# Optimization experiments

Measured on AMD Instinct MI355X. Metric: run time of the kernel, lower is better.

## Reference

```python
import jax, jax.numpy as jnp
import numpy as np

B, S, D, H, E, K, F = 1, 1024, 1024, 16, 8, 2, 4096


def setup_inputs() -> dict:
    key = jax.random.key(0)
    ks = jax.random.split(key, 8)
    n = lambda k, shape, sc: (jax.random.normal(k, shape, dtype=jnp.float32) * sc)
    return {
        "x": n(ks[0], (B, S, D), 1.0),
        "w_qkv": n(ks[1], (D, 3 * D), D ** -0.5),
        "w_o": n(ks[2], (D, D), D ** -0.5),
        "g1": jnp.ones((D,), jnp.float32),
        "b1": jnp.zeros((D,), jnp.float32),
        "wg": n(ks[3], (D, E), D ** -0.5),
        "w1": n(ks[4], (E, D, F), D ** -0.5),
        "bb1": jnp.zeros((E, F), jnp.float32),
        "w2": n(ks[5], (E, F, D), F ** -0.5),
        "bb2": jnp.zeros((E, D), jnp.float32),
        "g2": jnp.ones((D,), jnp.float32),
        "b2": jnp.zeros((D,), jnp.float32),
    }


def layernorm(x, g, b, eps=1e-5):
    m = x.mean(-1, keepdims=True)
    v = ((x - m) ** 2).mean(-1, keepdims=True)
    return (x - m) * jax.lax.rsqrt(v + eps) * g + b


def reference(x, w_qkv, w_o, g1, b1, wg, w1, bb1, w2, bb2, g2, b2):
    b, s, d = x.shape
    hd = d // H
    # --- multi-head causal self-attention ---
    qkv = x @ w_qkv  # [b,s,3d]
    q, k, v = jnp.split(qkv, 3, axis=-1)
    to_heads = lambda t: t.reshape(b, s, H, hd).transpose(0, 2, 1, 3)  # [b,h,s,hd]
    q, k, v = to_heads(q), to_heads(k), to_heads(v)
    scores = jnp.einsum("bhqd,bhkd->bhqk", q, k) / jnp.sqrt(jnp.float32(hd))
    causal = jnp.tril(jnp.ones((s, s), bool))
    scores = jnp.where(causal, scores, jnp.finfo(scores.dtype).min)
    attn = jax.nn.softmax(scores, axis=-1)
    o = jnp.einsum("bhqk,bhkd->bhqd", attn, v)
    o = o.transpose(0, 2, 1, 3).reshape(b, s, d) @ w_o
    # --- add & norm ---
    h = layernorm(x + o, g1, b1)
    # --- MoE FFN: softmax router, top-k, renormalized combine ---
    probs = jax.nn.softmax(h @ wg, axis=-1)  # [b,s,E]
    topv, topi = jax.lax.top_k(probs, K)
    topv = topv / topv.sum(-1, keepdims=True)
    w = (topv[..., None] * jax.nn.one_hot(topi, E, dtype=h.dtype)).sum(-2)  # [b,s,E]
    h1 = jax.nn.gelu(jnp.einsum("bsd,edf->ebsf", h, w1) + bb1[:, None, None, :])
    y = jnp.einsum("ebsf,efd->ebsd", h1, w2) + bb2[:, None, None, :]
    moe = jnp.einsum("ebsd,bse->bsd", y, w)
    # --- residual + norm of MoE block ---
    return layernorm(h + moe, g2, b2)
```

## Files before the change

kernel.cpp:

```cpp
#include <hip/hip_runtime.h>
#include <hip/hip_bf16.h>
#include <math.h>

#define SEQ 1024
#define DIM 1024
#define NH  16
#define NE  8
#define FF  4096

typedef float f32x4 __attribute__((ext_vector_type(4)));
typedef float f32x2 __attribute__((ext_vector_type(2)));
typedef short short8 __attribute__((ext_vector_type(8)));
typedef short s16x4 __attribute__((ext_vector_type(4)));

#define WAIT_VM(N) asm volatile("s_waitcnt vmcnt(" #N ")" ::: "memory")

__device__ __forceinline__ ushort f2bf(float f) {
  union { float f; unsigned u; } v; v.f = f;
  unsigned r = v.u + 0x7FFF + ((v.u >> 16) & 1);
  return (ushort)(r >> 16);
}
__device__ __forceinline__ float bf2f(ushort h) {
  union { unsigned u; float f; } v; v.u = ((unsigned)h) << 16;
  return v.f;
}

__device__ __forceinline__ float gelu_tanh(float x) {
  return 0.5f * x * (1.f + tanhf(0.7978845608028654f * (x + 0.044715f * x * x * x)));
}
__device__ __forceinline__ float gelu_fast(float x) {
  float u = 1.5957691216057308f * (x + 0.044715f * x * x * x);
  return x / (1.f + __expf(-u));
}

__device__ __forceinline__ void gl2lds16(const void* g, void* l) {
  __builtin_amdgcn_global_load_lds(
      (const __attribute__((address_space(1))) unsigned int*)g,
      (__attribute__((address_space(3))) unsigned int*)l, 16, 0, 0);
}

__global__ __launch_bounds__(256) void wconv_kernel(
    const float* __restrict__ wq, const float* __restrict__ wo,
    ushort* __restrict__ wqT, ushort* __restrict__ wqTl,
    ushort* __restrict__ woT, ushort* __restrict__ woTl) {
  __shared__ __align__(16) ushort th[64 * 64];
  __shared__ __align__(16) ushort tl[64 * 64];
  int z = blockIdx.z, t = threadIdx.x;
  const float* src; ushort* dh; ushort* dl; int R, C, r0, c0;
  if (z == 0) {
    src = wq; dh = wqT; dl = wqTl;
    R = DIM; C = 3 * DIM; r0 = blockIdx.y * 64; c0 = blockIdx.x * 64;
  } else {
    if (blockIdx.x >= 16) return;
    src = wo; dh = woT; dl = woTl;
    R = DIM; C = DIM; r0 = blockIdx.y * 64; c0 = blockIdx.x * 64;
  }
  int ry = (t >> 4) * 4;
  int cx = (t & 15) * 4;
  f32x4 v[4];
#pragma unroll
  for (int j = 0; j < 4; j++)
    v[j] = *(const f32x4*)&src[(size_t)(r0 + ry + j) * C + c0 + cx];
#pragma unroll
  for (int i = 0; i < 4; i++) {
    int trow = cx + i;
    int o = trow * 64 + (((ry >> 3) ^ (trow & 7)) << 3) + (ry & 7);
    ushort uh[4], ul[4];
#pragma unroll
    for (int j = 0; j < 4; j++) {
      float f = v[j][i];
      ushort hh = f2bf(f);
      uh[j] = hh;
      ul[j] = f2bf(f - bf2f(hh));
    }
    *(s16x4*)&th[o] = *(const s16x4*)uh;
    *(s16x4*)&tl[o] = *(const s16x4*)ul;
  }
  __syncthreads();
  int tr = t >> 2, tc = (t & 3) * 16;
  int b0 = (tc >> 3) ^ (tr & 7);
  int b1 = ((tc >> 3) + 1) ^ (tr & 7);
  size_t dbase = (size_t)(c0 + tr) * R + r0 + tc;
  short8 u0 = *(const short8*)&th[tr * 64 + b0 * 8];
  short8 u1 = *(const short8*)&th[tr * 64 + b1 * 8];
  *(short8*)&dh[dbase] = u0;
  *(short8*)&dh[dbase + 8] = u1;
  short8 l0 = *(const short8*)&tl[tr * 64 + b0 * 8];
  short8 l1 = *(const short8*)&tl[tr * 64 + b1 * 8];
  *(short8*)&dl[dbase] = l0;
  *(short8*)&dl[dbase + 8] = l1;
}

__global__ __launch_bounds__(256) void bfsplit_kernel(const float* __restrict__ in,
                                                      ushort* __restrict__ oh,
                                                      ushort* __restrict__ ol) {
  int i = (blockIdx.x * 256 + threadIdx.x) * 4;
  f32x4 v = *(const f32x4*)&in[i];
  ushort h[4], l[4];
#pragma unroll
  for (int j = 0; j < 4; j++) { h[j] = f2bf(v[j]); l[j] = f2bf(v[j] - bf2f(h[j])); }
  *(s16x4*)&oh[i] = *(const s16x4*)h;
  *(s16x4*)&ol[i] = *(const s16x4*)l;
}

#define MM_FEXP_LOAD(ra0v, ra1v, rb0v, rb1v, rb2v, rb3v, T)            \
  { int _ko = (T) * 32;                                                \
    ra0v = *(const short8*)(aG[0] + _ko);                              \
    ra1v = *(const short8*)(aG[1] + _ko);                              \
    rb0v = *(const f32x4*)(bG + (size_t)(_ko + 0) * N);                \
    rb1v = *(const f32x4*)(bG + (size_t)(_ko + 1) * N);                \
    rb2v = *(const f32x4*)(bG + (size_t)(_ko + 2) * N);                \
    rb3v = *(const f32x4*)(bG + (size_t)(_ko + 3) * N); }

#define MM_FEXP_STAGE(buf, ra0v, ra1v, rb0v, rb1v, rb2v, rb3v)         \
  { *(short8*)&As[buf][aw[0]] = ra0v;                                  \
    *(short8*)&As[buf][aw[1]] = ra1v;                                  \
    _Pragma("unroll")                                                  \
    for (int i = 0; i < 4; i++) {                                      \
      ushort u[4];                                                     \
      u[0] = f2bf(rb0v[i]); u[1] = f2bf(rb1v[i]);                      \
      u[2] = f2bf(rb2v[i]); u[3] = f2bf(rb3v[i]);                      \
      *(s16x4*)&Bs[buf][(nb * 4 + i) * 40 + bslot * 4] = *(const s16x4*)u; } }

#define MM_FEXP_MFMA(buf)                                              \
  { short8 af[4], bf[4];                                               \
    _Pragma("unroll")                                                  \
    for (int mi = 0; mi < 4; mi++) af[mi] = *(const short8*)&As[buf][aro[mi]]; \
    _Pragma("unroll")                                                  \
    for (int ni = 0; ni < 4; ni++) bf[ni] = *(const short8*)&Bs[buf][bro[ni]]; \
    _Pragma("unroll")                                                  \
    for (int mi = 0; mi < 4; mi++)                                     \
      _Pragma("unroll")                                                \
      for (int ni = 0; ni < 4; ni++)                                   \
        acc[mi][ni] = __builtin_amdgcn_mfma_f32_16x16x32_bf16(af[mi], bf[ni], acc[mi][ni], 0, 0, 0); }

template <int EPI, int KSPLIT>
__global__ __launch_bounds__(256) void mm_fexp(
    const ushort* __restrict__ A, const float* __restrict__ Bf,
    const float* __restrict__ bias, void* __restrict__ Cout,
    const int* __restrict__ tok, const int* __restrict__ offcnt,
    int N, int K)
{
  int zz = blockIdx.z;
  int e  = (KSPLIT > 1) ? (zz & (NE - 1)) : zz;
  int ks = (KSPLIT > 1) ? (zz >> 3) : 0;
  int off = offcnt[e], cnt = offcnt[NE + e];
  int m0 = blockIdx.y * 128;
  if (m0 >= cnt) return;
  int n0 = blockIdx.x * 128;
  const float* Bp = Bf + (size_t)e * K * N;
  const int Kc = K / KSPLIT, kbase = ks * Kc;

  __shared__ __align__(16) ushort As[2][128 * 32];
  __shared__ __align__(16) ushort Bs[2][128 * 40];

  int t = threadIdx.x, lane = t & 63, w = t >> 6, wr = w >> 1, wc = w & 1;

  const ushort* aG[2]; int aw[2];
#pragma unroll
  for (int c = 0; c < 2; c++) {
    int gid = w * 128 + c * 64 + lane;
    int m = gid >> 2, p = gid & 3;
    int kg = p ^ ((m >> 1) & 3);
    int mc = m0 + m; if (mc > cnt - 1) mc = cnt - 1;
    int arow = tok ? tok[off + mc] : (off + mc);
    aG[c] = A + (size_t)arow * K + kbase + kg * 8;
    aw[c] = gid * 8;
  }

  int kb = t >> 5, nb = t & 31;
  const float* bG = Bp + (size_t)(kbase + kb * 4) * N + n0 + nb * 4;
  int bslot = kb ^ ((nb & 3) << 1);

  int aro[4], bro[4];
#pragma unroll
  for (int mi = 0; mi < 4; mi++) {
    int m = wr * 64 + mi * 16 + (lane & 15);
    aro[mi] = (m * 4 + ((lane >> 4) ^ ((m >> 1) & 3))) * 8;
  }
#pragma unroll
  for (int ni = 0; ni < 4; ni++) {
    int n = wc * 64 + ni * 16 + (lane & 15);
    bro[ni] = n * 40 + ((((lane >> 4) * 2) ^ (((n >> 2) & 3) << 1))) * 4;
  }

  f32x4 acc[4][4] = {};
  const int nt = Kc / 32;

  short8 raA0, raA1, raB0, raB1;
  f32x4 rbA0, rbA1, rbA2, rbA3, rbB0, rbB1, rbB2, rbB3;
  MM_FEXP_LOAD(raA0, raA1, rbA0, rbA1, rbA2, rbA3, 0);
  MM_FEXP_LOAD(raB0, raB1, rbB0, rbB1, rbB2, rbB3, 1);

  for (int tt = 0; tt < nt; tt += 2) {
    MM_FEXP_STAGE(0, raA0, raA1, rbA0, rbA1, rbA2, rbA3);
    if (tt + 2 < nt) MM_FEXP_LOAD(raA0, raA1, rbA0, rbA1, rbA2, rbA3, tt + 2);
    asm volatile("s_waitcnt lgkmcnt(0)" ::: "memory");
    __builtin_amdgcn_sched_barrier(0);
    __builtin_amdgcn_s_barrier();
    MM_FEXP_MFMA(0);
    MM_FEXP_STAGE(1, raB0, raB1, rbB0, rbB1, rbB2, rbB3);
    if (tt + 3 < nt) MM_FEXP_LOAD(raB0, raB1, rbB0, rbB1, rbB2, rbB3, tt + 3);
    asm volatile("s_waitcnt lgkmcnt(0)" ::: "memory");
    __builtin_amdgcn_sched_barrier(0);
    __builtin_amdgcn_s_barrier();
    MM_FEXP_MFMA(1);
  }

  const float* biasp = (EPI == 3) ? nullptr : bias + (size_t)e * N;
  float* Cp = (float*)Cout + (size_t)ks * 2048 * N;
#pragma unroll
  for (int mi = 0; mi < 4; mi++) {
#pragma unroll
    for (int j = 0; j < 4; j++) {
      int grow = m0 + wr * 64 + mi * 16 + (lane >> 4) * 4 + j;
      if (grow >= cnt) continue;
      size_t rbase = (size_t)(off + grow) * N;
#pragma unroll
      for (int ni = 0; ni < 4; ni++) {
        int gcol = n0 + wc * 64 + ni * 16 + (lane & 15);
        float v = acc[mi][ni][j];
        if (EPI == 1) ((ushort*)Cout)[rbase + gcol] = f2bf(gelu_fast(v + biasp[gcol]));
        else          Cp[rbase + gcol] = v;
      }
    }
  }
}

#undef MM_FEXP_LOAD
#undef MM_FEXP_STAGE
#undef MM_FEXP_MFMA

__global__ __launch_bounds__(256) void mm_split(
    const ushort* __restrict__ Ah, const ushort* __restrict__ Al,
    const ushort* __restrict__ Bh, const ushort* __restrict__ Bl,
    float* __restrict__ C, int N, int K)
{
  int m0 = blockIdx.y * 128;
  int n0 = blockIdx.x * 128;

  __shared__ __align__(16) ushort Ahs[2][4096], Als[2][4096];
  __shared__ __align__(16) ushort Bhs[2][4096], Bls[2][4096];

  int t = threadIdx.x, lane = t & 63, w = t >> 6, wr = w >> 1, wc = w & 1;

  const ushort *aGh[2], *aGl[2], *bGh[2], *bGl[2];
  int lofs[2];
#pragma unroll
  for (int c = 0; c < 2; c++) {
    int gid = w * 128 + c * 64 + lane;
    int m = gid >> 2, p = gid & 3;
    int kg = p ^ ((m >> 1) & 3);
    aGh[c] = Ah + (size_t)(m0 + m) * K + kg * 8;
    aGl[c] = Al + (size_t)(m0 + m) * K + kg * 8;
    bGh[c] = Bh + (size_t)(n0 + m) * K + kg * 8;
    bGl[c] = Bl + (size_t)(n0 + m) * K + kg * 8;
    lofs[c] = (w * 128 + c * 64) * 8;
  }

  int aro[4], bro[4];
#pragma unroll
  for (int mi = 0; mi < 4; mi++) {
    int m = wr * 64 + mi * 16 + (lane & 15);
    aro[mi] = (m * 4 + ((lane >> 4) ^ ((m >> 1) & 3))) * 8;
  }
#pragma unroll
  for (int ni = 0; ni < 4; ni++) {
    int n = wc * 64 + ni * 16 + (lane & 15);
    bro[ni] = (n * 4 + ((lane >> 4) ^ ((n >> 1) & 3))) * 8;
  }

  f32x4 acc[4][4] = {};
  const int nt = K / 32;

#pragma unroll
  for (int c = 0; c < 2; c++) {
    gl2lds16(aGh[c], &Ahs[0][lofs[c]]); gl2lds16(aGl[c], &Als[0][lofs[c]]);
    gl2lds16(bGh[c], &Bhs[0][lofs[c]]); gl2lds16(bGl[c], &Bls[0][lofs[c]]);
  }
  if (nt > 1) {
#pragma unroll
    for (int c = 0; c < 2; c++) {
      gl2lds16(aGh[c] + 32, &Ahs[1][lofs[c]]); gl2lds16(aGl[c] + 32, &Als[1][lofs[c]]);
      gl2lds16(bGh[c] + 32, &Bhs[1][lofs[c]]); gl2lds16(bGl[c] + 32, &Bls[1][lofs[c]]);
    }
  }

  for (int tt = 0; tt < nt; tt++) {
    if (tt + 1 < nt) WAIT_VM(8); else WAIT_VM(0);
    __builtin_amdgcn_s_barrier();
    int b = tt & 1;
    short8 ah[4], al_[4], bh[4], bl_[4];
#pragma unroll
    for (int mi = 0; mi < 4; mi++) {
      ah[mi] = *(const short8*)&Ahs[b][aro[mi]];
      al_[mi] = *(const short8*)&Als[b][aro[mi]];
    }
#pragma unroll
    for (int ni = 0; ni < 4; ni++) {
      bh[ni] = *(const short8*)&Bhs[b][bro[ni]];
      bl_[ni] = *(const short8*)&Bls[b][bro[ni]];
    }
#pragma unroll
    for (int mi = 0; mi < 4; mi++)
#pragma unroll
      for (int ni = 0; ni < 4; ni++) {
        acc[mi][ni] = __builtin_amdgcn_mfma_f32_16x16x32_bf16(al_[mi], bh[ni], acc[mi][ni], 0, 0, 0);
        acc[mi][ni] = __builtin_amdgcn_mfma_f32_16x16x32_bf16(ah[mi], bl_[ni], acc[mi][ni], 0, 0, 0);
        acc[mi][ni] = __builtin_amdgcn_mfma_f32_16x16x32_bf16(ah[mi], bh[ni], acc[mi][ni], 0, 0, 0);
      }
    asm volatile("s_waitcnt lgkmcnt(0)" ::: "memory");
    __builtin_amdgcn_sched_barrier(0);
    __builtin_amdgcn_s_barrier();
    if (tt + 2 < nt) {
      int ko = (tt + 2) * 32;
#pragma unroll
      for (int c = 0; c < 2; c++) {
        gl2lds16(aGh[c] + ko, &Ahs[b][lofs[c]]); gl2lds16(aGl[c] + ko, &Als[b][lofs[c]]);
        gl2lds16(bGh[c] + ko, &Bhs[b][lofs[c]]); gl2lds16(bGl[c] + ko, &Bls[b][lofs[c]]);
      }
    }
  }

#pragma unroll
  for (int mi = 0; mi < 4; mi++)
#pragma unroll
    for (int j = 0; j < 4; j++) {
      int grow = m0 + wr * 64 + mi * 16 + (lane >> 4) * 4 + j;
      size_t rbase = (size_t)grow * N;
#pragma unroll
      for (int ni = 0; ni < 4; ni++) {
        int gcol = n0 + wc * 64 + ni * 16 + (lane & 15);
        C[rbase + gcol] = acc[mi][ni][j];
      }
    }
}

template <int EPI, int SPLIT>
__global__ __launch_bounds__(256) void mm_bf16(
    const float* __restrict__ A, const float* __restrict__ B,
    const float* __restrict__ bias, float* __restrict__ C,
    const int* __restrict__ tok, const int* __restrict__ offcnt,
    int M, int N, int K)
{
  int e = blockIdx.z;
  int off = 0, cnt = M;
  if (offcnt) { off = offcnt[e]; cnt = offcnt[NE + e]; }
  int m0 = blockIdx.y * 128;
  if (m0 >= cnt) return;
  const float* Bp = B + (size_t)e * K * N;
  const float* biasp = (EPI == 0) ? nullptr : bias + (size_t)e * N;
  int n0 = blockIdx.x * 128;

  __shared__ __align__(16) ushort As[(SPLIT + 1) * 128 * 32];
  __shared__ __align__(16) ushort Bs[(SPLIT + 1) * 128 * 32];

  int t = threadIdx.x;
  int lane = t & 63;
  int w = t >> 6, wr = w >> 1, wc = w & 1;

  const float* aptr[2];
  int aws[2];
  for (int i = 0; i < 2; i++) {
    int mr = i * 64 + (t >> 2);
    int mc = m0 + mr; if (mc > cnt - 1) mc = cnt - 1;
    int arow = tok ? tok[off + mc] : (off + mc);
    aptr[i] = A + (size_t)arow * K + (t & 3) * 8;
    aws[i] = mr * 32 + (t & 3) * 8;
  }

  int bn = t >> 1, bkh = (t & 1) * 16;
  const float* bptr = Bp + (size_t)bkh * N + n0 + bn;
  int bws0 = bn * 32 + 8 * (((bkh >> 3) + 0) ^ (bn & 3));
  int bws1 = bn * 32 + 8 * (((bkh >> 3) + 1) ^ (bn & 3));

  int aro[4], bro[4];
#pragma unroll
  for (int mi = 0; mi < 4; mi++)
    aro[mi] = (wr * 64 + mi * 16 + (lane & 15)) * 32 + (lane >> 4) * 8;
#pragma unroll
  for (int ni = 0; ni < 4; ni++) {
    int n = wc * 64 + ni * 16 + (lane & 15);
    bro[ni] = n * 32 + 8 * ((lane >> 4) ^ (n & 3));
  }

  f32x4 acc[4][4] = {};

  for (int k0 = 0; k0 < K; k0 += 32) {
#pragma unroll
    for (int i = 0; i < 2; i++) {
      f32x4 v0 = *(const f32x4*)(aptr[i] + k0);
      f32x4 v1 = *(const f32x4*)(aptr[i] + k0 + 4);
      ushort uh[8], ul[8];
#pragma unroll
      for (int j = 0; j < 4; j++) {
        float f0 = v0[j], f1 = v1[j];
        ushort h0 = f2bf(f0), h1 = f2bf(f1);
        uh[j] = h0; uh[4 + j] = h1;
        if (SPLIT) { ul[j] = f2bf(f0 - bf2f(h0)); ul[4 + j] = f2bf(f1 - bf2f(h1)); }
      }
      *(short8*)&As[aws[i]] = *(const short8*)uh;
      if (SPLIT) *(short8*)&As[4096 + aws[i]] = *(const short8*)ul;
    }
    {
      const float* bp = bptr + (size_t)k0 * N;
      ushort uh[16], ul[16];
#pragma unroll
      for (int i = 0; i < 16; i++) {
        float f = bp[(size_t)i * N];
        ushort h = f2bf(f);
        uh[i] = h;
        if (SPLIT) ul[i] = f2bf(f - bf2f(h));
      }
      *(short8*)&Bs[bws0] = *(const short8*)&uh[0];
      *(short8*)&Bs[bws1] = *(const short8*)&uh[8];
      if (SPLIT) {
        *(short8*)&Bs[4096 + bws0] = *(const short8*)&ul[0];
        *(short8*)&Bs[4096 + bws1] = *(const short8*)&ul[8];
      }
    }
    __syncthreads();
    short8 afh[4], bfh[4], afl[4], bfl[4];
#pragma unroll
    for (int mi = 0; mi < 4; mi++) {
      afh[mi] = *(const short8*)&As[aro[mi]];
      if (SPLIT) afl[mi] = *(const short8*)&As[4096 + aro[mi]];
    }
#pragma unroll
    for (int ni = 0; ni < 4; ni++) {
      bfh[ni] = *(const short8*)&Bs[bro[ni]];
      if (SPLIT) bfl[ni] = *(const short8*)&Bs[4096 + bro[ni]];
    }
#pragma unroll
    for (int mi = 0; mi < 4; mi++)
#pragma unroll
      for (int ni = 0; ni < 4; ni++) {
        if (SPLIT) {
          acc[mi][ni] = __builtin_amdgcn_mfma_f32_16x16x32_bf16(afl[mi], bfh[ni], acc[mi][ni], 0, 0, 0);
          acc[mi][ni] = __builtin_amdgcn_mfma_f32_16x16x32_bf16(afh[mi], bfl[ni], acc[mi][ni], 0, 0, 0);
        }
        acc[mi][ni] = __builtin_amdgcn_mfma_f32_16x16x32_bf16(afh[mi], bfh[ni], acc[mi][ni], 0, 0, 0);
      }
    __syncthreads();
  }

#pragma unroll
  for (int mi = 0; mi < 4; mi++) {
#pragma unroll
    for (int j = 0; j < 4; j++) {
      int grow = m0 + wr * 64 + mi * 16 + (lane >> 4) * 4 + j;
      if (grow >= cnt) continue;
      size_t rbase = (size_t)(off + grow) * N;
#pragma unroll
      for (int ni = 0; ni < 4; ni++) {
        int gcol = n0 + wc * 64 + ni * 16 + (lane & 15);
        float v = acc[mi][ni][j];
        if (EPI >= 1) v += biasp[gcol];
        if (EPI == 1) v = gelu_tanh(v);
        C[rbase + gcol] = v;
      }
    }
  }
}

__device__ __forceinline__ int vidx(int d, int key) {
  return d * 64 + ((((key >> 3) ^ (d & 7)) << 3) | (key & 7));
}

__global__ __launch_bounds__(256, 1) void attn_mfma(const float* __restrict__ qkv,
                                                    float* __restrict__ opart,
                                                    float* __restrict__ ml) {
  const int qb = blockIdx.x;
  const int ch = blockIdx.y;
  const int head = blockIdx.z;
  const int q0 = qb * 128;
  const int t = threadIdx.x;
  const int lane = t & 63, w = t >> 6;
  const int g = lane >> 4, l4 = lane & 15;

  __shared__ __align__(16) ushort Kh[64 * 64], Kl[64 * 64];
  __shared__ __align__(16) ushort Vh[64 * 64], Vl[64 * 64];
  __shared__ __align__(16) ushort Ph[4][32 * 72], Pl[4][32 * 72];

  short8 qh[2][2], ql[2][2];
#pragma unroll
  for (int mi = 0; mi < 2; mi++)
#pragma unroll
    for (int ks = 0; ks < 2; ks++) {
      int row = q0 + w * 32 + mi * 16 + l4;
      const float* qp = qkv + (size_t)row * 3072 + head * 64 + ks * 32 + g * 8;
      f32x4 a = *(const f32x4*)qp;
      f32x4 b4 = *(const f32x4*)(qp + 4);
      ushort uh[8], ul_[8];
#pragma unroll
      for (int j = 0; j < 4; j++) {
        ushort h0 = f2bf(a[j]), h1 = f2bf(b4[j]);
        uh[j] = h0; uh[4 + j] = h1;
        ul_[j] = f2bf(a[j] - bf2f(h0)); ul_[4 + j] = f2bf(b4[j] - bf2f(h1));
      }
      qh[mi][ks] = *(const short8*)uh;
      ql[mi][ks] = *(const short8*)ul_;
    }

  float m_s[2][4], l_s[2][4];
  f32x4 O[2][4] = {};
#pragma unroll
  for (int mi = 0; mi < 2; mi++)
#pragma unroll
    for (int j = 0; j < 4; j++) { m_s[mi][j] = -1e30f; l_s[mi][j] = 0.f; }

  const int kt_beg = ch ? (qb + 1) : 0;
  const int kt_end = ch ? 2 * (qb + 1) : (qb + 1);
  for (int kt = kt_beg; kt < kt_end; kt++) {
    const int kv0 = kt * 64;
    __syncthreads();
    {
      int key = t >> 2;
      int dblk = (t & 3) * 16;
      const float* kp = qkv + (size_t)(kv0 + key) * 3072 + 1024 + head * 64 + dblk;
      const float* vp = kp + 1024;
      f32x4 k0 = *(const f32x4*)kp, k1 = *(const f32x4*)(kp + 4),
            k2 = *(const f32x4*)(kp + 8), k3 = *(const f32x4*)(kp + 12);
      f32x4 v0 = *(const f32x4*)vp, v1 = *(const f32x4*)(vp + 4),
            v2 = *(const f32x4*)(vp + 8), v3 = *(const f32x4*)(vp + 12);
      float kf[16] = {k0[0],k0[1],k0[2],k0[3], k1[0],k1[1],k1[2],k1[3],
                      k2[0],k2[1],k2[2],k2[3], k3[0],k3[1],k3[2],k3[3]};
      float vf[16] = {v0[0],v0[1],v0[2],v0[3], v1[0],v1[1],v1[2],v1[3],
                      v2[0],v2[1],v2[2],v2[3], v3[0],v3[1],v3[2],v3[3]};
#pragma unroll
      for (int half = 0; half < 2; half++) {
        int d8 = (dblk >> 3) + half;
        int idx = key * 64 + ((d8 ^ (key & 7)) << 3);
        ushort uh[8], ul_[8];
#pragma unroll
        for (int j = 0; j < 8; j++) {
          float f = kf[half * 8 + j];
          ushort h = f2bf(f);
          uh[j] = h; ul_[j] = f2bf(f - bf2f(h));
        }
        *(short8*)&Kh[idx] = *(const short8*)uh;
        *(short8*)&Kl[idx] = *(const short8*)ul_;
      }
#pragma unroll
      for (int i = 0; i < 16; i++) {
        int d = dblk + i;
        int idx = vidx(d, key);
        float f = vf[i];
        ushort h = f2bf(f);
        Vh[idx] = h; Vl[idx] = f2bf(f - bf2f(h));
      }
    }
    __syncthreads();

    if (kv0 <= q0 + w * 32 + 31) {
      f32x4 S[2][4] = {};
#pragma unroll
      for (int ks = 0; ks < 2; ks++) {
        short8 kbh[4], kbl[4];
#pragma unroll
        for (int ni = 0; ni < 4; ni++) {
          int key = ni * 16 + l4;
          int d8 = ks * 4 + g;
          int idx = key * 64 + ((d8 ^ (key & 7)) << 3);
          kbh[ni] = *(const short8*)&Kh[idx];
          kbl[ni] = *(const short8*)&Kl[idx];
        }
#pragma unroll
        for (int mi = 0; mi < 2; mi++)
#pragma unroll
          for (int ni = 0; ni < 4; ni++) {
            S[mi][ni] = __builtin_amdgcn_mfma_f32_16x16x32_bf16(ql[mi][ks], kbh[ni], S[mi][ni], 0, 0, 0);
            S[mi][ni] = __builtin_amdgcn_mfma_f32_16x16x32_bf16(qh[mi][ks], kbl[ni], S[mi][ni], 0, 0, 0);
            S[mi][ni] = __builtin_amdgcn_mfma_f32_16x16x32_bf16(qh[mi][ks], kbh[ni], S[mi][ni], 0, 0, 0);
          }
      }
#pragma unroll
      for (int mi = 0; mi < 2; mi++) {
        int rowb = q0 + w * 32 + mi * 16 + g * 4;
        float mx[4] = {-1e30f, -1e30f, -1e30f, -1e30f};
#pragma unroll
        for (int ni = 0; ni < 4; ni++) {
          int col = kv0 + ni * 16 + l4;
#pragma unroll
          for (int j = 0; j < 4; j++) {
            float s = S[mi][ni][j] * 0.125f;
            if (col > rowb + j) s = -1e30f;
            S[mi][ni][j] = s;
            mx[j] = fmaxf(mx[j], s);
          }
        }
#pragma unroll
        for (int j = 0; j < 4; j++) {
#pragma unroll
          for (int msk = 8; msk; msk >>= 1) mx[j] = fmaxf(mx[j], __shfl_xor(mx[j], msk));
          float mn = fmaxf(m_s[mi][j], mx[j]);
          float sc = __expf(m_s[mi][j] - mn);
          m_s[mi][j] = mn;
          l_s[mi][j] *= sc;
#pragma unroll
          for (int df = 0; df < 4; df++) O[mi][df][j] *= sc;
        }
        float ps[4] = {0.f, 0.f, 0.f, 0.f};
#pragma unroll
        for (int ni = 0; ni < 4; ni++)
#pragma unroll
          for (int j = 0; j < 4; j++) {
            float p = __expf(S[mi][ni][j] - m_s[mi][j]);
            ps[j] += p;
            int rl = mi * 16 + g * 4 + j, cl = ni * 16 + l4;
            ushort h = f2bf(p);
            Ph[w][rl * 72 + cl] = h;
            Pl[w][rl * 72 + cl] = f2bf(p - bf2f(h));
          }
#pragma unroll
        for (int j = 0; j < 4; j++) {
#pragma unroll
          for (int msk = 8; msk; msk >>= 1) ps[j] += __shfl_xor(ps[j], msk);
          l_s[mi][j] += ps[j];
        }
      }
      asm volatile("s_waitcnt lgkmcnt(0)" ::: "memory");
      __builtin_amdgcn_sched_barrier(0);
#pragma unroll
      for (int ks = 0; ks < 2; ks++) {
        short8 pah[2], pal[2], vbh[4], vbl[4];
#pragma unroll
        for (int mi = 0; mi < 2; mi++) {
          int idx = (mi * 16 + l4) * 72 + ks * 32 + g * 8;
          pah[mi] = *(const short8*)&Ph[w][idx];
          pal[mi] = *(const short8*)&Pl[w][idx];
        }
#pragma unroll
        for (int df = 0; df < 4; df++) {
          int d = df * 16 + l4;
          int k8 = ks * 4 + g;
          int idx = d * 64 + ((k8 ^ (d & 7)) << 3);
          vbh[df] = *(const short8*)&Vh[idx];
          vbl[df] = *(const short8*)&Vl[idx];
        }
#pragma unroll
        for (int mi = 0; mi < 2; mi++)
#pragma unroll
          for (int df = 0; df < 4; df++) {
            O[mi][df] = __builtin_amdgcn_mfma_f32_16x16x32_bf16(pal[mi], vbh[df], O[mi][df], 0, 0, 0);
            O[mi][df] = __builtin_amdgcn_mfma_f32_16x16x32_bf16(pah[mi], vbl[df], O[mi][df], 0, 0, 0);
            O[mi][df] = __builtin_amdgcn_mfma_f32_16x16x32_bf16(pah[mi], vbh[df], O[mi][df], 0, 0, 0);
          }
      }
    }
  }

#pragma unroll
  for (int mi = 0; mi < 2; mi++)
#pragma unroll
    for (int j = 0; j < 4; j++) {
      int row = q0 + w * 32 + mi * 16 + g * 4 + j;
      if (l4 == 0) {
        float* mlp = ml + (((size_t)ch * NH + head) * SEQ + row) * 2;
        mlp[0] = m_s[mi][j];
        mlp[1] = l_s[mi][j];
      }
#pragma unroll
      for (int df = 0; df < 4; df++)
        opart[(size_t)ch * (SEQ * DIM) + (size_t)row * DIM + head * 64 + df * 16 + l4] =
            O[mi][df][j];
    }
}

__global__ __launch_bounds__(256) void attn_combine(const float* __restrict__ opart,
                                                    const float* __restrict__ ml,
                                                    float* __restrict__ o) {
  int row = blockIdx.x, t = threadIdx.x;
  int d0 = t * 4;
  int head = d0 >> 6;
  const float* p0 = ml + (((size_t)0 * NH + head) * SEQ + row) * 2;
  const float* p1 = ml + (((size_t)1 * NH + head) * SEQ + row) * 2;
  float m0 = p0[0], l0 = p0[1], m1 = p1[0], l1 = p1[1];
  float M = fmaxf(m0, m1);
  float w0 = __expf(m0 - M), w1 = __expf(m1 - M);
  float inv = 1.f / (l0 * w0 + l1 * w1);
  f32x4 O0 = *(const f32x4*)&opart[(size_t)row * DIM + d0];
  f32x4 O1 = *(const f32x4*)&opart[(size_t)(SEQ * DIM) + (size_t)row * DIM + d0];
  f32x4 r;
#pragma unroll
  for (int j = 0; j < 4; j++) r[j] = (O0[j] * w0 + O1[j] * w1) * inv;
  *(f32x4*)&o[(size_t)row * DIM + d0] = r;
}

__device__ float block_reduce_256(float v, float* red, int t) {
  red[t] = v; __syncthreads();
  for (int st = 128; st > 0; st >>= 1) {
    if (t < st) red[t] += red[t + st];
    __syncthreads();
  }
  float r = red[0];
  __syncthreads();
  return r;
}

__global__ __launch_bounds__(256) void addln_kernel(const float* __restrict__ x,
                                                    const float* __restrict__ r,
                                                    const float* __restrict__ g,
                                                    const float* __restrict__ b,
                                                    float* __restrict__ out,
                                                    ushort* __restrict__ outb) {
  __shared__ float red[256];
  int row = blockIdx.x, t = threadIdx.x;
  float vals[4];
  float s = 0.f;
  for (int i = 0; i < 4; i++) {
    int d = t + i * 256;
    vals[i] = x[(size_t)row * DIM + d] + r[(size_t)row * DIM + d];
    s += vals[i];
  }
  float mean = block_reduce_256(s, red, t) * (1.f / DIM);
  float vs = 0.f;
  for (int i = 0; i < 4; i++) { float d = vals[i] - mean; vs += d * d; }
  float var = block_reduce_256(vs, red, t) * (1.f / DIM);
  float inv = rsqrtf(var + 1e-5f);
  for (int i = 0; i < 4; i++) {
    int d = t + i * 256;
    float v = (vals[i] - mean) * inv * g[d] + b[d];
    out[(size_t)row * DIM + d] = v;
    if (outb) outb[(size_t)row * DIM + d] = f2bf(v);
  }
}

__global__ __launch_bounds__(256) void router_kernel(const float* __restrict__ h,
                                                     const float* __restrict__ wg,
                                                     int* __restrict__ topi,
                                                     float* __restrict__ topw) {
  __shared__ float red[NE][256];
  int tkn = blockIdx.x, t = threadIdx.x;
  float acc[NE] = {};
  for (int i = 0; i < 4; i++) {
    int d = t + i * 256;
    float hv = h[(size_t)tkn * DIM + d];
    const float* wr = wg + (size_t)d * NE;
    for (int e = 0; e < NE; e++) acc[e] += hv * wr[e];
  }
  for (int e = 0; e < NE; e++) red[e][t] = acc[e];
  __syncthreads();
  for (int st = 128; st > 0; st >>= 1) {
    if (t < st)
      for (int e = 0; e < NE; e++) red[e][t] += red[e][t + st];
    __syncthreads();
  }
  if (t == 0) {
    float l[NE];
    for (int e = 0; e < NE; e++) l[e] = red[e][0];
    int i0 = 0;
    for (int e = 1; e < NE; e++) if (l[e] > l[i0]) i0 = e;
    int i1 = -1;
    for (int e = 0; e < NE; e++) {
      if (e == i0) continue;
      if (i1 < 0 || l[e] > l[i1]) i1 = e;
    }
    float p1 = __expf(l[i1] - l[i0]);
    float inv = 1.f / (1.f + p1);
    topi[tkn * 2] = i0; topi[tkn * 2 + 1] = i1;
    topw[tkn * 2] = inv; topw[tkn * 2 + 1] = p1 * inv;
  }
}

__global__ __launch_bounds__(1024) void compact_kernel(const int* __restrict__ topi,
                                                       int* __restrict__ tok,
                                                       int* __restrict__ assign_row,
                                                       int* __restrict__ offcnt) {
  __shared__ int scan[1024];
  __shared__ int sbase;
  int t = threadIdx.x;
  if (t == 0) sbase = 0;
  __syncthreads();
  for (int e = 0; e < NE; e++) {
    int which = -1;
    if (topi[t * 2] == e) which = 0;
    else if (topi[t * 2 + 1] == e) which = 1;
    scan[t] = (which >= 0) ? 1 : 0;
    __syncthreads();
    for (int s2 = 1; s2 < 1024; s2 <<= 1) {
      int add = (t >= s2) ? scan[t - s2] : 0;
      __syncthreads();
      scan[t] += add;
      __syncthreads();
    }
    int incl = scan[t];
    int total = scan[1023];
    int base = sbase;
    if (which >= 0) {
      int pos = base + incl - 1;
      tok[pos] = t;
      assign_row[t * 2 + which] = pos;
    }
    if (t == 0) { offcnt[e] = base; offcnt[NE + e] = total; }
    __syncthreads();
    if (t == 0) sbase = base + total;
    __syncthreads();
  }
}

template <int KS>
__global__ __launch_bounds__(256) void final_ln_kernel(const float* __restrict__ h,
                                                       const float* __restrict__ y,
                                                       const int* __restrict__ assign_row,
                                                       const float* __restrict__ topw,
                                                       const int* __restrict__ topi,
                                                       const float* __restrict__ bb2,
                                                       const float* __restrict__ g,
                                                       const float* __restrict__ b,
                                                       float* __restrict__ out) {
  __shared__ float red[256];
  int row = blockIdx.x, t = threadIdx.x;
  int r0 = assign_row[row * 2], r1 = assign_row[row * 2 + 1];
  float w0 = topw[row * 2], w1 = topw[row * 2 + 1];
  float vals[4];
  float s = 0.f;
  for (int i = 0; i < 4; i++) {
    int d = t + i * 256;
    float acc0 = 0.f, acc1 = 0.f;
#pragma unroll
    for (int p = 0; p < KS; p++) {
      acc0 += y[(size_t)p * 2048 * DIM + (size_t)r0 * DIM + d];
      acc1 += y[(size_t)p * 2048 * DIM + (size_t)r1 * DIM + d];
    }
    float v = h[(size_t)row * DIM + d] + w0 * acc0 + w1 * acc1;
    if (KS > 1) {
      int e0 = topi[row * 2], e1 = topi[row * 2 + 1];
      v += w0 * bb2[e0 * DIM + d] + w1 * bb2[e1 * DIM + d];
    }
    vals[i] = v;
    s += v;
  }
  float mean = block_reduce_256(s, red, t) * (1.f / DIM);
  float vs = 0.f;
  for (int i = 0; i < 4; i++) { float d = vals[i] - mean; vs += d * d; }
  float var = block_reduce_256(vs, red, t) * (1.f / DIM);
  float inv = rsqrtf(var + 1e-5f);
  for (int i = 0; i < 4; i++) {
    int d = t + i * 256;
    out[(size_t)row * DIM + d] = (vals[i] - mean) * inv * g[d] + b[d];
  }
}

extern "C" void kernel_launch(void* const* d_in, const int* in_sizes, int n_in,
                              void* d_out, int out_size, void* d_ws, size_t ws_size,
                              hipStream_t stream) {
  const float* x     = (const float*)d_in[0];
  const float* w_qkv = (const float*)d_in[1];
  const float* w_o   = (const float*)d_in[2];
  const float* g1    = (const float*)d_in[3];
  const float* b1    = (const float*)d_in[4];
  const float* wg    = (const float*)d_in[5];
  const float* w1    = (const float*)d_in[6];
  const float* bb1   = (const float*)d_in[7];
  const float* w2    = (const float*)d_in[8];
  const float* bb2   = (const float*)d_in[9];
  const float* g2    = (const float*)d_in[10];
  const float* b2    = (const float*)d_in[11];
  float* out = (float*)d_out;
  float* ws = (float*)d_ws;

  const bool fast = ws_size >= (size_t)46671872 * 4;

  if (fast) {
    float* qkv    = ws;
    float* attn_o = ws + 3145728;
    float* oproj  = ws + 4194304;
    float* h      = ws + 5242880;
    float* ybuf   = ws + 6291456;
    float* topw   = ws + 8388608;
    int*   ibase  = (int*)(ws + 8390656);
    int* topi       = ibase;
    int* tok        = ibase + 2048;
    int* assign_row = ibase + 4096;
    int* offcnt     = ibase + 6144;
    ushort* hb  = (ushort*)(ws + 8398848);
    ushort* h1b = (ushort*)(ws + 8923136);
    ushort* wqT  = (ushort*)(ws + 13117440);
    ushort* wqTl = wqT + 3145728;
    ushort* woT  = wqT + 6291456;
    ushort* woTl = wqT + 7340032;
    float* ypart = ws + 17311744;
    ushort* xh = (ushort*)ybuf;
    ushort* xl = xh + 1048576;
    ushort* oh = xh + 2097152;
    ushort* ol = xh + 3145728;
    float* opart = ypart;
    float* mlbuf = ypart + 2097152;

    wconv_kernel<<<dim3(48, 16, 2), 256, 0, stream>>>(w_qkv, w_o,
                                                      wqT, wqTl, woT, woTl);
    bfsplit_kernel<<<dim3(SEQ * DIM / 1024), 256, 0, stream>>>(x, xh, xl);
    mm_split<<<dim3(24, 8), 256, 0, stream>>>(xh, xl, wqT, wqTl, qkv, 3 * DIM, DIM);
    attn_mfma<<<dim3(8, 2, NH), 256, 0, stream>>>(qkv, opart, mlbuf);
    attn_combine<<<dim3(SEQ), 256, 0, stream>>>(opart, mlbuf, attn_o);
    bfsplit_kernel<<<dim3(SEQ * DIM / 1024), 256, 0, stream>>>(attn_o, oh, ol);
    mm_split<<<dim3(8, 8), 256, 0, stream>>>(oh, ol, woT, woTl, oproj, DIM, DIM);
    addln_kernel<<<dim3(SEQ), 256, 0, stream>>>(x, oproj, g1, b1, h, hb);
    router_kernel<<<dim3(SEQ), 256, 0, stream>>>(h, wg, topi, topw);
    compact_kernel<<<dim3(1), 1024, 0, stream>>>(topi, tok, assign_row, offcnt);
    mm_fexp<1, 1><<<dim3(FF / 128, 8, NE), 256, 0, stream>>>(hb, w1, bb1, (void*)h1b,
                                                             tok, offcnt, FF, DIM);
    mm_fexp<3, 4><<<dim3(DIM / 128, 8, NE * 4), 256, 0, stream>>>(h1b, w2, nullptr,
                                                                  (void*)ypart,
                                                                  nullptr, offcnt, DIM, FF);
    final_ln_kernel<4><<<dim3(SEQ), 256, 0, stream>>>(h, ypart, assign_row, topw,
                                                      topi, bb2, g2, b2, out);
  } else {
    float* qkv    = ws;
    float* attn_o = ws + 3145728;
    float* oproj  = ws + 4194304;
    float* h      = ws + 5242880;
    float* h1     = ws + 6291456;
    float* ybuf   = ws + 14680064;
    float* topw   = ws + 16777216;
    int*   ibase  = (int*)(ws + 16779264);
    int* topi       = ibase;
    int* tok        = ibase + 2048;
    int* assign_row = ibase + 4096;
    int* offcnt     = ibase + 6144;
    float* opart = h1;
    float* mlbuf = h1 + 2097152;

    mm_bf16<0, 1><<<dim3(24, 8, 1), 256, 0, stream>>>(x, w_qkv, nullptr, qkv,
                                                      nullptr, nullptr, SEQ, 3 * DIM, DIM);
    attn_mfma<<<dim3(8, 2, NH), 256, 0, stream>>>(qkv, opart, mlbuf);
    attn_combine<<<dim3(SEQ), 256, 0, stream>>>(opart, mlbuf, attn_o);
    mm_bf16<0, 1><<<dim3(8, 8, 1), 256, 0, stream>>>(attn_o, w_o, nullptr, oproj,
                                                     nullptr, nullptr, SEQ, DIM, DIM);
    addln_kernel<<<dim3(SEQ), 256, 0, stream>>>(x, oproj, g1, b1, h, nullptr);
    router_kernel<<<dim3(SEQ), 256, 0, stream>>>(h, wg, topi, topw);
    compact_kernel<<<dim3(1), 1024, 0, stream>>>(topi, tok, assign_row, offcnt);
    mm_bf16<1, 0><<<dim3(32, 8, NE), 256, 0, stream>>>(h, w1, bb1, h1,
                                                       tok, offcnt, SEQ, FF, DIM);
    mm_bf16<2, 0><<<dim3(8, 8, NE), 256, 0, stream>>>(h1, w2, bb2, ybuf,
                                                      nullptr, offcnt, SEQ, DIM, FF);
    final_ln_kernel<1><<<dim3(SEQ), 256, 0, stream>>>(h, ybuf, assign_row, topw,
                                                      nullptr, nullptr, g2, b2, out);
  }
}
```

Baseline: 313.5 us.

## Split attention KV range into four chunks and fuse combine, split, and router kernels

Attention now splits each query block's causal KV range into four chunks instead of two, so the launch has more blocks and per-block work is more even. The combine kernel merges four partials and, on the fast path, writes the bf16 hi/lo split directly, which removes a separate bfsplit launch and an fp32 round trip. LayerNorm and the router are fused into one kernel that computes the gate logits and top-2 in the same block. The costs are more partial-output memory traffic, an extra reduction over eight experts per row, and a top-2 computed from logits rather than softmax probabilities, which gives the same ranking and weights.

```diff
diff --git a/kernel.cpp b/kernel.cpp
--- a/kernel.cpp
+++ b/kernel.cpp
@@ -7,6 +7,7 @@
 #define NH  16
 #define NE  8
 #define FF  4096
+#define NCH 4
 
 typedef float f32x4 __attribute__((ext_vector_type(4)));
 typedef float f32x2 __attribute__((ext_vector_type(2)));
@@ -509,8 +510,9 @@
 #pragma unroll
     for (int j = 0; j < 4; j++) { m_s[mi][j] = -1e30f; l_s[mi][j] = 0.f; }
 
-  const int kt_beg = ch ? (qb + 1) : 0;
-  const int kt_end = ch ? 2 * (qb + 1) : (qb + 1);
+  const int ntot = 2 * (qb + 1);
+  const int kt_beg = (ch * ntot) / NCH;
+  const int kt_end = ((ch + 1) * ntot) / NCH;
   for (int kt = kt_beg; kt < kt_end; kt++) {
     const int kv0 = kt * 64;
     __syncthreads();
@@ -667,24 +669,46 @@
     }
 }
 
+template <int SPLIT>
 __global__ __launch_bounds__(256) void attn_combine(const float* __restrict__ opart,
                                                     const float* __restrict__ ml,
-                                                    float* __restrict__ o) {
+                                                    float* __restrict__ o,
+                                                    ushort* __restrict__ oh,
+                                                    ushort* __restrict__ ol) {
   int row = blockIdx.x, t = threadIdx.x;
   int d0 = t * 4;
   int head = d0 >> 6;
-  const float* p0 = ml + (((size_t)0 * NH + head) * SEQ + row) * 2;
-  const float* p1 = ml + (((size_t)1 * NH + head) * SEQ + row) * 2;
-  float m0 = p0[0], l0 = p0[1], m1 = p1[0], l1 = p1[1];
-  float M = fmaxf(m0, m1);
-  float w0 = __expf(m0 - M), w1 = __expf(m1 - M);
-  float inv = 1.f / (l0 * w0 + l1 * w1);
-  f32x4 O0 = *(const f32x4*)&opart[(size_t)row * DIM + d0];
-  f32x4 O1 = *(const f32x4*)&opart[(size_t)(SEQ * DIM) + (size_t)row * DIM + d0];
-  f32x4 r;
-#pragma unroll
-  for (int j = 0; j < 4; j++) r[j] = (O0[j] * w0 + O1[j] * w1) * inv;
-  *(f32x4*)&o[(size_t)row * DIM + d0] = r;
+  float m[NCH], l[NCH];
+#pragma unroll
+  for (int ch = 0; ch < NCH; ch++) {
+    const float* p = ml + (((size_t)ch * NH + head) * SEQ + row) * 2;
+    m[ch] = p[0]; l[ch] = p[1];
+  }
+  float M = m[0];
+#pragma unroll
+  for (int ch = 1; ch < NCH; ch++) M = fmaxf(M, m[ch]);
+  float wgt[NCH], den = 0.f;
+#pragma unroll
+  for (int ch = 0; ch < NCH; ch++) { wgt[ch] = __expf(m[ch] - M); den += l[ch] * wgt[ch]; }
+  float inv = 1.f / den;
+  f32x4 r = {0.f, 0.f, 0.f, 0.f};
+#pragma unroll
+  for (int ch = 0; ch < NCH; ch++) {
+    f32x4 O = *(const f32x4*)&opart[(size_t)ch * (SEQ * DIM) + (size_t)row * DIM + d0];
+#pragma unroll
+    for (int j = 0; j < 4; j++) r[j] += O[j] * wgt[ch];
+  }
+#pragma unroll
+  for (int j = 0; j < 4; j++) r[j] *= inv;
+  if (SPLIT) {
+    ushort hh[4], ll[4];
+#pragma unroll
+    for (int j = 0; j < 4; j++) { hh[j] = f2bf(r[j]); ll[j] = f2bf(r[j] - bf2f(hh[j])); }
+    *(s16x4*)&oh[(size_t)row * DIM + d0] = *(const s16x4*)hh;
+    *(s16x4*)&ol[(size_t)row * DIM + d0] = *(const s16x4*)ll;
+  } else {
+    *(f32x4*)&o[(size_t)row * DIM + d0] = r;
+  }
 }
 
 __device__ float block_reduce_256(float v, float* red, int t) {
@@ -696,6 +720,65 @@
   float r = red[0];
   __syncthreads();
   return r;
+}
+
+__global__ __launch_bounds__(256) void addln_router_kernel(
+    const float* __restrict__ x, const float* __restrict__ r,
+    const float* __restrict__ g, const float* __restrict__ b,
+    const float* __restrict__ wg,
+    float* __restrict__ out, ushort* __restrict__ outb,
+    int* __restrict__ topi, float* __restrict__ topw) {
+  __shared__ float red[256];
+  __shared__ float red2[NE][256];
+  int row = blockIdx.x, t = threadIdx.x;
+  float vals[4];
+  float s = 0.f;
+  for (int i = 0; i < 4; i++) {
+    int d = t + i * 256;
+    vals[i] = x[(size_t)row * DIM + d] + r[(size_t)row * DIM + d];
+    s += vals[i];
+  }
+  float mean = block_reduce_256(s, red, t) * (1.f / DIM);
+  float vs = 0.f;
+  for (int i = 0; i < 4; i++) { float d = vals[i] - mean; vs += d * d; }
+  float var = block_reduce_256(vs, red, t) * (1.f / DIM);
+  float inv = rsqrtf(var + 1e-5f);
+  float hv4[4];
+  for (int i = 0; i < 4; i++) {
+    int d = t + i * 256;
+    float v = (vals[i] - mean) * inv * g[d] + b[d];
+    hv4[i] = v;
+    out[(size_t)row * DIM + d] = v;
+    outb[(size_t)row * DIM + d] = f2bf(v);
+  }
+  float acc[NE] = {};
+  for (int i = 0; i < 4; i++) {
+    int d = t + i * 256;
+    const float* wr = wg + (size_t)d * NE;
+    for (int e = 0; e < NE; e++) acc[e] += hv4[i] * wr[e];
+  }
+  for (int e = 0; e < NE; e++) red2[e][t] = acc[e];
+  __syncthreads();
+  for (int st = 128; st > 0; st >>= 1) {
+    if (t < st)
+      for (int e = 0; e < NE; e++) red2[e][t] += red2[e][t + st];
+    __syncthreads();
+  }
+  if (t == 0) {
+    float l[NE];
+    for (int e = 0; e < NE; e++) l[e] = red2[e][0];
+    int i0 = 0;
+    for (int e = 1; e < NE; e++) if (l[e] > l[i0]) i0 = e;
+    int i1 = -1;
+    for (int e = 0; e < NE; e++) {
+      if (e == i0) continue;
+      if (i1 < 0 || l[e] > l[i1]) i1 = e;
+    }
+    float p1 = __expf(l[i1] - l[i0]);
+    float iv = 1.f / (1.f + p1);
+    topi[row * 2] = i0; topi[row * 2 + 1] = i1;
+    topw[row * 2] = iv; topw[row * 2 + 1] = p1 * iv;
+  }
 }
 
 __global__ __launch_bounds__(256) void addln_kernel(const float* __restrict__ x,
@@ -864,7 +947,6 @@
 
   if (fast) {
     float* qkv    = ws;
-    float* attn_o = ws + 3145728;
     float* oproj  = ws + 4194304;
     float* h      = ws + 5242880;
     float* ybuf   = ws + 6291456;
@@ -886,18 +968,17 @@
     ushort* oh = xh + 2097152;
     ushort* ol = xh + 3145728;
     float* opart = ypart;
-    float* mlbuf = ypart + 2097152;
+    float* mlbuf = ypart + NCH * 1048576;
 
     wconv_kernel<<<dim3(48, 16, 2), 256, 0, stream>>>(w_qkv, w_o,
                                                       wqT, wqTl, woT, woTl);
     bfsplit_kernel<<<dim3(SEQ * DIM / 1024), 256, 0, stream>>>(x, xh, xl);
     mm_split<<<dim3(24, 8), 256, 0, stream>>>(xh, xl, wqT, wqTl, qkv, 3 * DIM, DIM);
-    attn_mfma<<<dim3(8, 2, NH), 256, 0, stream>>>(qkv, opart, mlbuf);
-    attn_combine<<<dim3(SEQ), 256, 0, stream>>>(opart, mlbuf, attn_o);
-    bfsplit_kernel<<<dim3(SEQ * DIM / 1024), 256, 0, stream>>>(attn_o, oh, ol);
+    attn_mfma<<<dim3(8, NCH, NH), 256, 0, stream>>>(qkv, opart, mlbuf);
+    attn_combine<1><<<dim3(SEQ), 256, 0, stream>>>(opart, mlbuf, nullptr, oh, ol);
     mm_split<<<dim3(8, 8), 256, 0, stream>>>(oh, ol, woT, woTl, oproj, DIM, DIM);
-    addln_kernel<<<dim3(SEQ), 256, 0, stream>>>(x, oproj, g1, b1, h, hb);
-    router_kernel<<<dim3(SEQ), 256, 0, stream>>>(h, wg, topi, topw);
+    addln_router_kernel<<<dim3(SEQ), 256, 0, stream>>>(x, oproj, g1, b1, wg,
+                                                       h, hb, topi, topw);
     compact_kernel<<<dim3(1), 1024, 0, stream>>>(topi, tok, assign_row, offcnt);
     mm_fexp<1, 1><<<dim3(FF / 128, 8, NE), 256, 0, stream>>>(hb, w1, bb1, (void*)h1b,
                                                              tok, offcnt, FF, DIM);
@@ -920,12 +1001,12 @@
     int* assign_row = ibase + 4096;
     int* offcnt     = ibase + 6144;
     float* opart = h1;
-    float* mlbuf = h1 + 2097152;
+    float* mlbuf = h1 + NCH * 1048576;
 
     mm_bf16<0, 1><<<dim3(24, 8, 1), 256, 0, stream>>>(x, w_qkv, nullptr, qkv,
                                                       nullptr, nullptr, SEQ, 3 * DIM, DIM);
-    attn_mfma<<<dim3(8, 2, NH), 256, 0, stream>>>(qkv, opart, mlbuf);
-    attn_combine<<<dim3(SEQ), 256, 0, stream>>>(opart, mlbuf, attn_o);
+    attn_mfma<<<dim3(8, NCH, NH), 256, 0, stream>>>(qkv, opart, mlbuf);
+    attn_combine<0><<<dim3(SEQ), 256, 0, stream>>>(opart, mlbuf, attn_o, nullptr, nullptr);
     mm_bf16<0, 1><<<dim3(8, 8, 1), 256, 0, stream>>>(attn_o, w_o, nullptr, oproj,
                                                      nullptr, nullptr, SEQ, DIM, DIM);
     addln_kernel<<<dim3(SEQ), 256, 0, stream>>>(x, oproj, g1, b1, h, nullptr);
```

New measurement: 312.7 us. No clear change (-0.3%).
